# Performance work log

Hardware: AMD Instinct MI355X
Metric: run time of the kernel (lower is better)

## Reference

```python
import jax, jax.numpy as jnp
import numpy as np

NUM_HEADS = 16
HEAD_DIM = 64
NUM_BUCKETS = 32
MAX_DIST = 128
EPS = 1e-5
SCALE = HEAD_DIM ** -0.5


def layer_norm(x, g, b):
    m = jnp.mean(x, axis=-1, keepdims=True)
    v = jnp.mean(jnp.square(x - m), axis=-1, keepdims=True)
    return (x - m) * jax.lax.rsqrt(v + EPS) * g + b


def rel_pos_bias(emb, num_q, num_k):
    # T5-style relative position bucketing (non-causal, bidirectional halves)
    i, j = num_q, num_k
    q_pos = jnp.arange(j - i, j)
    k_pos = jnp.arange(j)
    rel = k_pos[None, :] - q_pos[:, None]  # [i, j]
    nb = NUM_BUCKETS // 2
    ret = (rel >= 0).astype(jnp.int32) * nb
    n = jnp.abs(rel)
    max_exact = nb // 2
    val_large = max_exact + (
        jnp.log(jnp.maximum(n, 1).astype(jnp.float32) / max_exact)
        / np.log(MAX_DIST / max_exact) * (nb - max_exact)
    ).astype(jnp.int32)
    val_large = jnp.minimum(val_large, nb - 1)
    bucket = ret + jnp.where(n < max_exact, n, val_large)
    bias = emb[bucket]                       # [i, j, h]
    return jnp.transpose(bias, (2, 0, 1))[None]  # [1, h, i, j]


def attention(x, ctx, ng, nbv, ncg, ncb, wq, wkv, wo, bo, rel_emb):
    b, n, _ = x.shape
    m = ctx.shape[1]
    xn = layer_norm(x, ng, nbv)
    cn = layer_norm(ctx, ncg, ncb)
    q = xn @ wq                              # [b, n, mid]
    kv = cn @ wkv                            # [b, m, 2*mid]
    k, v = jnp.split(kv, 2, axis=-1)
    def heads(t, L):
        return t.reshape(b, L, NUM_HEADS, HEAD_DIM).transpose(0, 2, 1, 3)
    q, k, v = heads(q, n), heads(k, m), heads(v, m)
    sim = jnp.einsum('bhnd,bhmd->bhnm', q, k)
    sim = (sim + rel_pos_bias(rel_emb, n, m)) * SCALE  # bias added pre-scale (faithful)
    attn = jax.nn.softmax(sim, axis=-1)
    out = jnp.einsum('bhnm,bhmd->bhnd', attn, v)
    out = out.transpose(0, 2, 1, 3).reshape(b, n, NUM_HEADS * HEAD_DIM)
    return out @ wo + bo


def setup_inputs() -> dict:
    key = jax.random.key(0)
    ks = jax.random.split(key, 20)
    F, MID, CF = 1024, NUM_HEADS * HEAD_DIM, 1024
    w = lambda k, shape, s=0.02: jax.random.normal(k, shape, jnp.float32) * s
    inp = {
        'x': jax.random.normal(ks[0], (2, 2048, F), jnp.float32),
        'context': jax.random.normal(ks[1], (2, 512, CF), jnp.float32),
        # self-attention params
        'sa_norm_g': 1.0 + w(ks[2], (F,), 0.1), 'sa_norm_b': w(ks[3], (F,), 0.1),
        'sa_normc_g': 1.0 + w(ks[4], (F,), 0.1), 'sa_normc_b': w(ks[5], (F,), 0.1),
        'sa_wq': w(ks[6], (F, MID)), 'sa_wkv': w(ks[7], (F, 2 * MID)),
        'sa_wo': w(ks[8], (MID, F)), 'sa_bo': w(ks[9], (F,), 0.01),
        'sa_rel': w(ks[10], (NUM_BUCKETS, NUM_HEADS), 0.1),
        # cross-attention params
        'ca_norm_g': 1.0 + w(ks[11], (F,), 0.1), 'ca_norm_b': w(ks[12], (F,), 0.1),
        'ca_normc_g': 1.0 + w(ks[13], (CF,), 0.1), 'ca_normc_b': w(ks[14], (CF,), 0.1),
        'ca_wq': w(ks[15], (F, MID)), 'ca_wkv': w(ks[16], (CF, 2 * MID)),
        'ca_wo': w(ks[17], (MID, F)), 'ca_bo': w(ks[18], (F,), 0.01),
        'ca_rel': w(ks[19], (NUM_BUCKETS, NUM_HEADS), 0.1),
    }
    return inp


def reference(x, context,
              sa_norm_g, sa_norm_b, sa_normc_g, sa_normc_b,
              sa_wq, sa_wkv, sa_wo, sa_bo, sa_rel,
              ca_norm_g, ca_norm_b, ca_normc_g, ca_normc_b,
              ca_wq, ca_wkv, ca_wo, ca_bo, ca_rel):
    # self-attention (context = x, norm_context applied to x)
    x = attention(x, x, sa_norm_g, sa_norm_b, sa_normc_g, sa_normc_b,
                  sa_wq, sa_wkv, sa_wo, sa_bo, sa_rel) + x
    # cross-attention with residual
    x = attention(x, context, ca_norm_g, ca_norm_b, ca_normc_g, ca_normc_b,
                  ca_wq, ca_wkv, ca_wo, ca_bo, ca_rel) + x
    return x
```

## Files before the change

### kernel.cpp

```cpp
#include <hip/hip_runtime.h>
#include <hip/hip_bf16.h>

typedef __hip_bfloat16 bf16;
typedef __attribute__((ext_vector_type(8))) short bf16x8;
typedef __attribute__((ext_vector_type(4))) float f32x4;

__device__ __forceinline__ float b2f(bf16 v) { return __bfloat162float(v); }
__device__ __forceinline__ bf16 f2b(float v) { return __float2bfloat16(v); }

__device__ __forceinline__ float ldx(const void* p, size_t i, bool isb) {
    return isb ? b2f(((const bf16*)p)[i]) : ((const float*)p)[i];
}
__device__ __forceinline__ void stx(void* p, size_t i, bool isb, float v) {
    if (isb) ((bf16*)p)[i] = f2b(v);
    else     ((float*)p)[i] = v;
}
__device__ __forceinline__ void ldx8(const void* p, size_t i, bool isb, float* o) {
    if (isb) {
        const bf16x8 v = *(const bf16x8*)((const bf16*)p + i);
#pragma unroll
        for (int j = 0; j < 8; j++) o[j] = b2f(((const bf16*)&v)[j]);
    } else {
        const float4 v0 = *(const float4*)((const float*)p + i);
        const float4 v1 = *(const float4*)((const float*)p + i + 4);
        o[0]=v0.x; o[1]=v0.y; o[2]=v0.z; o[3]=v0.w;
        o[4]=v1.x; o[5]=v1.y; o[6]=v1.z; o[7]=v1.w;
    }
}

__global__ void sniff_kernel(const void* __restrict__ x, int* __restrict__ flag) {
    const unsigned* w = (const unsigned*)x;
    const int t = threadIdx.x;
    int cnt = 0;
#pragma unroll
    for (int i = 0; i < 4; i++) {
        const unsigned word = w[t * 4 + i];
        const int e = (word >> 23) & 0xFF;
        cnt += (e >= 192) ? 1 : 0;
    }
    __shared__ int red[4];
#pragma unroll
    for (int o = 32; o > 0; o >>= 1) cnt += __shfl_down(cnt, o);
    if ((t & 63) == 0) red[t >> 6] = cnt;
    __syncthreads();
    if (t == 0) flag[0] = ((red[0] + red[1] + red[2] + red[3]) >= 512) ? 1 : 0;
}

__global__ void wconv4_kernel(const void* __restrict__ Wq,
                              const void* __restrict__ Wkv,
                              const void* __restrict__ Wo,
                              bf16* __restrict__ WTq, bf16* __restrict__ WTkv,
                              bf16* __restrict__ WTo,
                              const int* __restrict__ flagp) {
    const bool isb = (*flagp != 0);
    const int z = blockIdx.z;
    const void* W = (z == 0) ? Wq : (z == 3) ? Wo : Wkv;
    bf16* Wt      = (z == 0) ? WTq : (z == 3) ? WTo : WTkv;
    const int N   = (z == 1 || z == 2) ? 2048 : 1024;
    const int K = 1024;
    __shared__ float T[64][65];
    const int n0 = blockIdx.x * 64 + ((z == 2) ? 1024 : 0);
    const int k0 = blockIdx.y * 64;
    const int t = threadIdx.x;
    const int rr = t >> 3, c8 = (t & 7) * 8;
#pragma unroll
    for (int i = 0; i < 2; i++) {
        const int row = rr + i * 32;
        float v[8];
        ldx8(W, (size_t)(k0 + row) * N + n0 + c8, isb, v);
#pragma unroll
        for (int j = 0; j < 8; j++) T[row][c8 + j] = v[j];
    }
    __syncthreads();
#pragma unroll
    for (int i = 0; i < 2; i++) {
        const int row = rr + i * 32;
        bf16x8 ov;
#pragma unroll
        for (int j = 0; j < 8; j++) ((bf16*)&ov)[j] = f2b(T[c8 + j][row]);
        *(bf16x8*)(Wt + (size_t)(n0 + row) * K + k0 + c8) = ov;
    }
}

__global__ void ln_dual_kernel(const void* __restrict__ in, size_t in_off, long in_bs,
                               int in_ext,
                               const void* __restrict__ g1, const void* __restrict__ b1,
                               const void* __restrict__ g2, const void* __restrict__ b2,
                               bf16* __restrict__ out1, bf16* __restrict__ out2,
                               long out_bs, const int* __restrict__ flagp) {
    const int F = 1024;
    const bool isb = (*flagp != 0);
    const bool inb = in_ext ? isb : true;
    const int row = blockIdx.x;
    const int z = blockIdx.z;
    const int t = threadIdx.x;
    const size_t base = in_off + (size_t)z * in_bs + (size_t)row * F;
    const size_t obase = (size_t)z * out_bs + (size_t)row * F;

    float v[4];
    float s = 0.f;
#pragma unroll
    for (int i = 0; i < 4; i++) { v[i] = ldx(in, base + t + 256 * i, inb); s += v[i]; }

    __shared__ float red1[4];
    __shared__ float red2[4];
#pragma unroll
    for (int o = 32; o > 0; o >>= 1) s += __shfl_down(s, o);
    if ((t & 63) == 0) red1[t >> 6] = s;
    __syncthreads();
    const float mean = (red1[0] + red1[1] + red1[2] + red1[3]) * (1.0f / F);

    float ss = 0.f;
#pragma unroll
    for (int i = 0; i < 4; i++) { float d = v[i] - mean; ss += d * d; }
#pragma unroll
    for (int o = 32; o > 0; o >>= 1) ss += __shfl_down(ss, o);
    if ((t & 63) == 0) red2[t >> 6] = ss;
    __syncthreads();
    const float var = (red2[0] + red2[1] + red2[2] + red2[3]) * (1.0f / F);
    const float rn = rsqrtf(var + 1e-5f);

#pragma unroll
    for (int i = 0; i < 4; i++) {
        const int idx = t + 256 * i;
        const float nv = (v[i] - mean) * rn;
        out1[obase + idx] = f2b(nv * ldx(g1, idx, isb) + ldx(b1, idx, isb));
        if (out2) out2[obase + idx] = f2b(nv * ldx(g2, idx, isb) + ldx(b2, idx, isb));
    }
}

struct GArgs {
    const bf16* A; const bf16* Bt; void* C;
    const void* bias; const void* res;
    bf16* kb0; bf16* kb1;
    int c_ext, res_ext, N, mode, zsplit, zrows, nbx, nby;
};

__global__ __launch_bounds__(256) void gemm_fused(GArgs ga, GArgs gb,
                                                  const int* __restrict__ flagp) {
    const bool sec = (int)blockIdx.x >= ga.nbx;
    const GArgs g = sec ? gb : ga;
    const int bx = (int)blockIdx.x - (sec ? ga.nbx : 0);
    const int by = (int)blockIdx.y;
    if (by >= g.nby) return;

    const int K = 1024;
    const bool isb = (*flagp != 0);

    __shared__ bf16 As[128][72];
    __shared__ bf16 Bs[128][72];

    const int t = threadIdx.x;
    const int w = t >> 6, lane = t & 63, li = lane & 15, quad = lane >> 4;
    const int wm = (w & 1) * 64, wn = (w >> 1) * 64;
    const int bm = by * 128, bn = bx * 128;

    f32x4 acc[4][4];
#pragma unroll
    for (int mi = 0; mi < 4; mi++)
#pragma unroll
        for (int ni = 0; ni < 4; ni++)
#pragma unroll
            for (int r = 0; r < 4; r++) acc[mi][ni][r] = 0.f;

    for (int k0 = 0; k0 < K; k0 += 64) {
#pragma unroll
        for (int c = 0; c < 4; c++) {
            const int d = c * 256 + t;
            const int row = d >> 3, ch = (d & 7) * 8;
            *(bf16x8*)&As[row][ch] = *(const bf16x8*)(g.A + (size_t)(bm + row) * K + k0 + ch);
            *(bf16x8*)&Bs[row][ch] = *(const bf16x8*)(g.Bt + (size_t)(bn + row) * K + k0 + ch);
        }
        __syncthreads();
#pragma unroll
        for (int kc = 0; kc < 2; kc++) {
            bf16x8 af[4], bfr[4];
#pragma unroll
            for (int i = 0; i < 4; i++) {
                af[i]  = *(const bf16x8*)&As[wm + i * 16 + li][kc * 32 + quad * 8];
                bfr[i] = *(const bf16x8*)&Bs[wn + i * 16 + li][kc * 32 + quad * 8];
            }
#pragma unroll
            for (int mi = 0; mi < 4; mi++)
#pragma unroll
                for (int ni = 0; ni < 4; ni++)
                    acc[mi][ni] = __builtin_amdgcn_mfma_f32_16x16x32_bf16(
                        af[mi], bfr[ni], acc[mi][ni], 0, 0, 0);
        }
        __syncthreads();
    }

    if (g.mode == 1) {
#pragma unroll
        for (int mi = 0; mi < 4; mi++)
#pragma unroll
            for (int r = 0; r < 4; r++) {
                const int row = bm + wm + mi * 16 + quad * 4 + r;
                bf16* kb = (row < g.zsplit) ? g.kb0 : g.kb1;
                const int lrow = (row < g.zsplit) ? row : row - g.zsplit;
#pragma unroll
                for (int ni = 0; ni < 4; ni++) {
                    const int col = bn + wn + ni * 16 + li;
                    const float v = acc[mi][ni][r];
                    if (col < 1024)
                        kb[(size_t)lrow * 1024 + col] = f2b(v);
                    else
                        kb[(size_t)1024 * g.zrows + (size_t)(col - 1024) * g.zrows + lrow] = f2b(v);
                }
            }
        return;
    }

#pragma unroll
    for (int mi = 0; mi < 4; mi++)
#pragma unroll
        for (int r = 0; r < 4; r++) {
            const int row = bm + wm + mi * 16 + quad * 4 + r;
#pragma unroll
            for (int ni = 0; ni < 4; ni++) {
                const int col = bn + wn + ni * 16 + li;
                float v = acc[mi][ni][r];
                if (g.bias) v += ldx(g.bias, col, isb);
                if (g.res)  v += ldx(g.res, (size_t)row * g.N + col, g.res_ext ? isb : true);
                stx(g.C, (size_t)row * g.N + col, g.c_ext ? isb : true, v);
            }
        }
}

__global__ __launch_bounds__(256) void gemm_mfma(
    const bf16* __restrict__ A, long a_bs, const void* __restrict__ W,
    void* __restrict__ C, size_t c_off, long c_bs, int c_ext,
    const void* __restrict__ bias,
    const void* __restrict__ res, size_t res_off, long res_bs, int res_ext,
    int K, int N, int mode, int R,
    bf16* __restrict__ kb0, bf16* __restrict__ kb1,
    const int* __restrict__ flagp) {

    const bool isb = (*flagp != 0);
    const bool resb = res_ext ? isb : true;
    const bool cb = c_ext ? isb : true;
    const int z = blockIdx.z;

    const bf16* Az = A + (size_t)z * a_bs;
    const size_t coz = c_off + (size_t)z * c_bs;
    const size_t roz = res_off + (size_t)z * res_bs;

    __shared__ bf16 As[64][72];
    __shared__ bf16 Bs[64][72];

    const int t = threadIdx.x;
    const int w = t >> 6, lane = t & 63, li = lane & 15, quad = lane >> 4;
    const int wm = (w & 1) * 32, wn = (w >> 1) * 32;
    const int bm = blockIdx.y * 64, bn = blockIdx.x * 64;

    f32x4 acc[2][2];
#pragma unroll
    for (int mi = 0; mi < 2; mi++)
#pragma unroll
        for (int ni = 0; ni < 2; ni++)
#pragma unroll
            for (int r = 0; r < 4; r++) acc[mi][ni][r] = 0.f;

    for (int k0 = 0; k0 < K; k0 += 64) {
#pragma unroll
        for (int c = 0; c < 2; c++) {
            const int lin = t * 16 + c * 8;
            const int row = lin >> 6, kk = lin & 63;
            *(bf16x8*)&As[row][kk] = *(const bf16x8*)(Az + (size_t)(bm + row) * K + k0 + kk);
        }
#pragma unroll
        for (int c = 0; c < 2; c++) {
            const int lin = t * 16 + c * 8;
            const int kk = lin >> 6, n0 = lin & 63;
            float v[8];
            ldx8(W, (size_t)(k0 + kk) * N + bn + n0, isb, v);
            const int st = t & 7;
#pragma unroll
            for (int i = 0; i < 8; i++) {
                const int ii = (i + st) & 7;
                Bs[n0 + ii][kk] = f2b(v[ii]);
            }
        }
        __syncthreads();
#pragma unroll
        for (int kc = 0; kc < 2; kc++) {
            bf16x8 af[2], bfr[2];
#pragma unroll
            for (int mi = 0; mi < 2; mi++)
                af[mi] = *(const bf16x8*)&As[wm + mi * 16 + li][kc * 32 + quad * 8];
#pragma unroll
            for (int ni = 0; ni < 2; ni++)
                bfr[ni] = *(const bf16x8*)&Bs[wn + ni * 16 + li][kc * 32 + quad * 8];
#pragma unroll
            for (int mi = 0; mi < 2; mi++)
#pragma unroll
                for (int ni = 0; ni < 2; ni++)
                    acc[mi][ni] = __builtin_amdgcn_mfma_f32_16x16x32_bf16(
                        af[mi], bfr[ni], acc[mi][ni], 0, 0, 0);
        }
        __syncthreads();
    }

    if (mode == 1) {
        bf16* kb = z ? kb1 : kb0;
#pragma unroll
        for (int mi = 0; mi < 2; mi++)
#pragma unroll
            for (int r = 0; r < 4; r++) {
                const int row = bm + wm + mi * 16 + quad * 4 + r;
#pragma unroll
                for (int ni = 0; ni < 2; ni++) {
                    const int col = bn + wn + ni * 16 + li;
                    const float v = acc[mi][ni][r];
                    if (col < 1024)
                        kb[(size_t)row * 1024 + col] = f2b(v);
                    else
                        kb[(size_t)1024 * R + (size_t)(col - 1024) * R + row] = f2b(v);
                }
            }
        return;
    }

#pragma unroll
    for (int mi = 0; mi < 2; mi++)
#pragma unroll
        for (int r = 0; r < 4; r++) {
            const int row = bm + wm + mi * 16 + quad * 4 + r;
#pragma unroll
            for (int ni = 0; ni < 2; ni++) {
                const int col = bn + wn + ni * 16 + li;
                float v = acc[mi][ni][r];
                if (bias) v += ldx(bias, col, isb);
                if (res)  v += ldx(res, roz + (size_t)row * N + col, resb);
                stx(C, coz + (size_t)row * N + col, cb, v);
            }
        }
}

__global__ __launch_bounds__(64) void attn_flash(
    const bf16* __restrict__ qb, const bf16* __restrict__ kv0,
    const bf16* __restrict__ kv1,
    const void* __restrict__ rel_emb, bf16* __restrict__ out,
    long qo_bs, long out_bs, int m, int rel_off, const int* __restrict__ flagp) {

    const float SC = 0.125f * 1.44269504f;
    const bool isb = (*flagp != 0);
    const int id = blockIdx.x;
    const int xcd = id & 7;
    const int slot = id >> 3;
    const int c = (slot >> 6) * 8 + xcd;
    const int h = c & 15, z = c >> 4;
    const int q0 = (slot & 63) * 32;
    const int t = threadIdx.x;
    const int li = t & 15, quad = t >> 4;

    const bf16* qz = qb + (size_t)z * qo_bs;
    bf16* oz = out + (size_t)z * out_bs;
    const bf16* kb = z ? kv1 : kv0;
    const bf16* vtb = kb + (size_t)m * 1024;

    __shared__ float bias_s[32];
    __shared__ float tab[2080];
    __shared__ bf16 Ps[16][40];

    if (t < 32) bias_s[t] = ldx(rel_emb, t * 16 + h, isb) * SC - 40.0f;
    __syncthreads();

    const int tsz = m + 31;
    for (int i = t; i < tsz; i += 64) {
        const int rel = i - 31 - q0 + rel_off;
        const int ab = rel < 0 ? -rel : rel;
        int bucket = rel >= 0 ? 16 : 0;
        if (ab < 8) {
            bucket += ab;
        } else {
            const int p = 31 - __clz(ab);
            const int k2 = 2 * p + ((ab * ab >= (1 << (2 * p + 1))) ? 1 : 0);
            const int val = k2 + 2;
            bucket += (val > 15) ? 15 : val;
        }
        tab[i] = bias_s[bucket];
    }
    __syncthreads();

    bf16x8 aq[2][2];
#pragma unroll
    for (int g = 0; g < 2; g++)
#pragma unroll
        for (int kc = 0; kc < 2; kc++)
            aq[g][kc] = *(const bf16x8*)(qz + (size_t)(q0 + g * 16 + li) * 1024
                                         + h * 64 + kc * 32 + quad * 8);

    bf16x8 ones;
#pragma unroll
    for (int j = 0; j < 8; j++) ((short*)&ones)[j] = 0x3F80;

    f32x4 o[2][4], lac[2];
#pragma unroll
    for (int g = 0; g < 2; g++) {
#pragma unroll
        for (int r = 0; r < 4; r++) lac[g][r] = 0.f;
#pragma unroll
        for (int nb = 0; nb < 4; nb++)
#pragma unroll
            for (int r = 0; r < 4; r++) o[g][nb][r] = 0.f;
    }

#define LOADKV(KF, VF, J)                                                      \
    {                                                                          \
        _Pragma("unroll")                                                      \
        for (int nb = 0; nb < 2; nb++)                                         \
            _Pragma("unroll")                                                  \
            for (int kc = 0; kc < 2; kc++)                                     \
                KF[nb * 2 + kc] = *(const bf16x8*)(                            \
                    kb + (size_t)((J) + nb * 16 + li) * 1024 + h * 64          \
                    + kc * 32 + quad * 8);                                     \
        _Pragma("unroll")                                                      \
        for (int nb = 0; nb < 4; nb++)                                         \
            VF[nb] = *(const bf16x8*)(                                         \
                vtb + (size_t)(h * 64 + nb * 16 + li) * m + (J) + quad * 8);   \
    }

#define ABODY(KF, VF, J0)                                                      \
    {                                                                          \
        _Pragma("unroll")                                                      \
        for (int g = 0; g < 2; g++) {                                          \
            f32x4 s[2];                                                        \
            __builtin_amdgcn_s_setprio(1);                                     \
            _Pragma("unroll")                                                  \
            for (int nb = 0; nb < 2; nb++) {                                   \
                f32x4 a;                                                       \
                _Pragma("unroll")                                              \
                for (int r = 0; r < 4; r++) a[r] = 0.f;                        \
                _Pragma("unroll")                                              \
                for (int kc = 0; kc < 2; kc++)                                 \
                    a = __builtin_amdgcn_mfma_f32_16x16x32_bf16(               \
                        aq[g][kc], KF[nb * 2 + kc], a, 0, 0, 0);               \
                s[nb] = a;                                                     \
            }                                                                  \
            __builtin_amdgcn_s_setprio(0);                                     \
            _Pragma("unroll")                                                  \
            for (int nb = 0; nb < 2; nb++)                                     \
                _Pragma("unroll")                                              \
                for (int r = 0; r < 4; r++) {                                  \
                    const int ti = (J0) + nb * 16 + li + 31                    \
                                   - (g * 16 + quad * 4 + r);                  \
                    s[nb][r] = exp2f(fmaf(s[nb][r], SC, tab[ti]));             \
                }                                                              \
            _Pragma("unroll")                                                  \
            for (int nb = 0; nb < 2; nb++)                                     \
                _Pragma("unroll")                                              \
                for (int r = 0; r < 4; r++)                                    \
                    Ps[quad * 4 + r][nb * 16 + li] = f2b(s[nb][r]);            \
            const bf16x8 ap = *(const bf16x8*)&Ps[li][quad * 8];               \
            __builtin_amdgcn_s_setprio(1);                                     \
            _Pragma("unroll")                                                  \
            for (int nb = 0; nb < 4; nb++)                                     \
                o[g][nb] = __builtin_amdgcn_mfma_f32_16x16x32_bf16(            \
                    ap, VF[nb], o[g][nb], 0, 0, 0);                            \
            lac[g] = __builtin_amdgcn_mfma_f32_16x16x32_bf16(                  \
                ap, ones, lac[g], 0, 0, 0);                                    \
            __builtin_amdgcn_s_setprio(0);                                     \
        }                                                                      \
    }

    bf16x8 kA[4], vA[4], kB[4], vB[4];
    LOADKV(kA, vA, 0);
    for (int j0 = 0; j0 < m; j0 += 64) {
        LOADKV(kB, vB, j0 + 32);
        ABODY(kA, vA, j0);
        const int jn = (j0 + 64 < m) ? (j0 + 64) : 0;
        LOADKV(kA, vA, jn);
        ABODY(kB, vB, j0 + 32);
    }

#undef LOADKV
#undef ABODY

#pragma unroll
    for (int g = 0; g < 2; g++)
#pragma unroll
        for (int r = 0; r < 4; r++) {
            const float inv = 1.0f / lac[g][r];
            const int qi = q0 + g * 16 + quad * 4 + r;
#pragma unroll
            for (int nb = 0; nb < 4; nb++)
                oz[(size_t)qi * 1024 + h * 64 + nb * 16 + li] = f2b(o[g][nb][r] * inv);
        }
}

extern "C" void kernel_launch(void* const* d_in, const int* in_sizes, int n_in,
                              void* d_out, int out_size, void* d_ws, size_t ws_size,
                              hipStream_t stream) {
    const long M1 = 1024 * 1024;
    const long M2 = 2 * 1024 * 1024;
    const long M4 = 4 * 1024 * 1024;
    if (ws_size < 24u * 1024 * 1024 + 256) return;

    const void* x      = d_in[0];
    const void* ctx    = d_in[1];
    const void* sa_ng  = d_in[2];
    const void* sa_nb  = d_in[3];
    const void* sa_ncg = d_in[4];
    const void* sa_ncb = d_in[5];
    const void* sa_wq  = d_in[6];
    const void* sa_wkv = d_in[7];
    const void* sa_wo  = d_in[8];
    const void* sa_bo  = d_in[9];
    const void* sa_rel = d_in[10];
    const void* ca_ng  = d_in[11];
    const void* ca_nb  = d_in[12];
    const void* ca_ncg = d_in[13];
    const void* ca_ncb = d_in[14];
    const void* ca_wq  = d_in[15];
    const void* ca_wkv = d_in[16];
    const void* ca_wo  = d_in[17];
    const void* ca_bo  = d_in[18];
    const void* ca_rel = d_in[19];

    int* flag = (int*)d_ws;
    bf16* F_A = (bf16*)((char*)d_ws + 256);
    bf16* F_B = F_A + M4;
    bf16* F_C = F_B + M4;
    bf16* WT  = F_C + M4;
    bf16* F_X = WT + M4;
    bf16* qd  = (bf16*)d_out;

    sniff_kernel<<<1, 256, 0, stream>>>(x, flag);

    if (ws_size >= 40u * 1024 * 1024 + 256) {
        bf16* WTq = WT;
        bf16* WTkv = WT + M1;
        bf16* WTo = WT + 3 * M1;
        GArgs gz = {};

        wconv4_kernel<<<dim3(16, 16, 4), 256, 0, stream>>>(
            sa_wq, sa_wkv, sa_wo, WTq, WTkv, WTo, flag);
        ln_dual_kernel<<<dim3(2048, 1, 2), 256, 0, stream>>>(
            x, 0, M2, 1, sa_ng, sa_nb, sa_ncg, sa_ncb, F_X, F_B, M2, flag);
        {
            GArgs gq = {};
            gq.A = F_X; gq.Bt = WTq; gq.C = qd;
            gq.N = 1024; gq.nbx = 8; gq.nby = 32;
            GArgs gkv = {};
            gkv.A = F_B; gkv.Bt = WTkv;
            gkv.N = 2048; gkv.mode = 1; gkv.zsplit = 2048; gkv.zrows = 2048;
            gkv.kb0 = F_A; gkv.kb1 = F_C; gkv.nbx = 16; gkv.nby = 32;
            gemm_fused<<<dim3(24, 32), 256, 0, stream>>>(gq, gkv, flag);
        }
        attn_flash<<<dim3(2048), 64, 0, stream>>>(
            qd, F_A, F_C, sa_rel, qd, M2, M2, 2048, 0, flag);
        {
            GArgs go = {};
            go.A = qd; go.Bt = WTo; go.C = F_B;
            go.bias = sa_bo; go.res = x; go.res_ext = 1;
            go.N = 1024; go.nbx = 8; go.nby = 32;
            gemm_fused<<<dim3(8, 32), 256, 0, stream>>>(go, gz, flag);
        }

        wconv4_kernel<<<dim3(16, 16, 4), 256, 0, stream>>>(
            ca_wq, ca_wkv, ca_wo, WTq, WTkv, WTo, flag);
        ln_dual_kernel<<<dim3(2048, 1, 2), 256, 0, stream>>>(
            F_B, 0, M2, 0, ca_ng, ca_nb, nullptr, nullptr, F_X, nullptr, M2, flag);
        ln_dual_kernel<<<dim3(512, 1, 2), 256, 0, stream>>>(
            ctx, 0, 512 * 1024, 1, ca_ncg, ca_ncb, nullptr, nullptr,
            F_C, nullptr, 512 * 1024, flag);
        {
            GArgs gq = {};
            gq.A = F_X; gq.Bt = WTq; gq.C = qd;
            gq.N = 1024; gq.nbx = 8; gq.nby = 32;
            GArgs gkv = {};
            gkv.A = F_C; gkv.Bt = WTkv;
            gkv.N = 2048; gkv.mode = 1; gkv.zsplit = 512; gkv.zrows = 512;
            gkv.kb0 = F_A; gkv.kb1 = F_A + M1; gkv.nbx = 16; gkv.nby = 8;
            gemm_fused<<<dim3(24, 32), 256, 0, stream>>>(gq, gkv, flag);
        }
        attn_flash<<<dim3(2048), 64, 0, stream>>>(
            qd, F_A, F_A + M1, ca_rel, F_C, M2, M2, 512, 1536, flag);
        {
            GArgs go = {};
            go.A = F_C; go.Bt = WTo; go.C = d_out; go.c_ext = 1;
            go.bias = ca_bo; go.res = F_B;
            go.N = 1024; go.nbx = 8; go.nby = 32;
            gemm_fused<<<dim3(8, 32), 256, 0, stream>>>(go, gz, flag);
        }
        return;
    }

    ln_dual_kernel<<<dim3(2048, 1, 2), 256, 0, stream>>>(
        x, 0, M2, 1, sa_ng, sa_nb, sa_ncg, sa_ncb, F_A, F_B, M2, flag);
    gemm_mfma<<<dim3(16, 32, 2), 256, 0, stream>>>(
        F_A, M2, sa_wq, qd, 0, M2, 0, nullptr, nullptr, 0, 0, 0,
        1024, 1024, 0, 0, nullptr, nullptr, flag);
    gemm_mfma<<<dim3(32, 32, 2), 256, 0, stream>>>(
        F_B, M2, sa_wkv, nullptr, 0, 0, 0, nullptr, nullptr, 0, 0, 0,
        1024, 2048, 1, 2048, F_A, F_C, flag);
    attn_flash<<<dim3(2048), 64, 0, stream>>>(
        qd, F_A, F_C, sa_rel, qd, M2, M2, 2048, 0, flag);
    gemm_mfma<<<dim3(16, 32, 2), 256, 0, stream>>>(
        qd, M2, sa_wo, F_B, 0, M2, 0, sa_bo, x, 0, M2, 1,
        1024, 1024, 0, 0, nullptr, nullptr, flag);

    ln_dual_kernel<<<dim3(2048, 1, 2), 256, 0, stream>>>(
        F_B, 0, M2, 0, ca_ng, ca_nb, nullptr, nullptr, F_A, nullptr, M2, flag);
    ln_dual_kernel<<<dim3(512, 1, 2), 256, 0, stream>>>(
        ctx, 0, 512 * 1024, 1, ca_ncg, ca_ncb, nullptr, nullptr,
        F_C, nullptr, 512 * 1024, flag);
    gemm_mfma<<<dim3(16, 32, 2), 256, 0, stream>>>(
        F_A, M2, ca_wq, qd, 0, M2, 0, nullptr, nullptr, 0, 0, 0,
        1024, 1024, 0, 0, nullptr, nullptr, flag);
    gemm_mfma<<<dim3(32, 8, 2), 256, 0, stream>>>(
        F_C, 512 * 1024, ca_wkv, nullptr, 0, 0, 0, nullptr, nullptr, 0, 0, 0,
        1024, 2048, 1, 512, F_A, F_A + M1, flag);
    attn_flash<<<dim3(2048), 64, 0, stream>>>(
        qd, F_A, F_A + M1, ca_rel, F_C, M2, M2, 512, 1536, flag);
    gemm_mfma<<<dim3(16, 32, 2), 256, 0, stream>>>(
        F_C, M2, ca_wo, d_out, 0, M2, 1, ca_bo, F_B, 0, M2, 0,
        1024, 1024, 0, 0, nullptr, nullptr, flag);
}
```

Before: 503.0 us.

## Hoist cross-attention weight conversion and context KV projection into first phase

Both attentions' weight transposes now happen in one 8-slice conversion launch, and the context layernorm plus cross-attention K/V projection move into the first fused GEMM launch alongside the self-attention Q/KV GEMMs. This cuts kernel launches and fills the GPU better in the first GEMM, leaving a smaller Q-only GEMM for the cross phase. The attention kernel also drops s_setprio hints and double-buffers the P scratch tile per group. It needs a larger workspace (56MB threshold), and if the workspace is smaller the code falls back to the slow path.

Result: faster. 489.3 us (-2.7%).

```diff
diff --git a/kernel.cpp b/kernel.cpp
--- a/kernel.cpp
+++ b/kernel.cpp
@@ -46,20 +46,29 @@
     if (t == 0) flag[0] = ((red[0] + red[1] + red[2] + red[3]) >= 512) ? 1 : 0;
 }
 
-__global__ void wconv4_kernel(const void* __restrict__ Wq,
+__global__ void wconv8_kernel(const void* __restrict__ Wq,
                               const void* __restrict__ Wkv,
                               const void* __restrict__ Wo,
+                              const void* __restrict__ Wq2,
+                              const void* __restrict__ Wkv2,
+                              const void* __restrict__ Wo2,
                               bf16* __restrict__ WTq, bf16* __restrict__ WTkv,
                               bf16* __restrict__ WTo,
+                              bf16* __restrict__ WTq2, bf16* __restrict__ WTkv2,
+                              bf16* __restrict__ WTo2,
                               const int* __restrict__ flagp) {
     const bool isb = (*flagp != 0);
     const int z = blockIdx.z;
-    const void* W = (z == 0) ? Wq : (z == 3) ? Wo : Wkv;
-    bf16* Wt      = (z == 0) ? WTq : (z == 3) ? WTo : WTkv;
-    const int N   = (z == 1 || z == 2) ? 2048 : 1024;
+    const int zz = z & 3;
+    const bool ca = z >= 4;
+    const void* W = ca ? ((zz == 0) ? Wq2 : (zz == 3) ? Wo2 : Wkv2)
+                       : ((zz == 0) ? Wq  : (zz == 3) ? Wo  : Wkv);
+    bf16* Wt      = ca ? ((zz == 0) ? WTq2 : (zz == 3) ? WTo2 : WTkv2)
+                       : ((zz == 0) ? WTq  : (zz == 3) ? WTo  : WTkv);
+    const int N   = (zz == 1 || zz == 2) ? 2048 : 1024;
     const int K = 1024;
     __shared__ float T[64][65];
-    const int n0 = blockIdx.x * 64 + ((z == 2) ? 1024 : 0);
+    const int n0 = blockIdx.x * 64 + ((zz == 2) ? 1024 : 0);
     const int k0 = blockIdx.y * 64;
     const int t = threadIdx.x;
     const int rr = t >> 3, c8 = (t & 7) * 8;
@@ -136,11 +145,13 @@
     int c_ext, res_ext, N, mode, zsplit, zrows, nbx, nby;
 };
 
-__global__ __launch_bounds__(256) void gemm_fused(GArgs ga, GArgs gb,
+__global__ __launch_bounds__(256) void gemm_fused(GArgs ga, GArgs gb, GArgs gc,
                                                   const int* __restrict__ flagp) {
-    const bool sec = (int)blockIdx.x >= ga.nbx;
-    const GArgs g = sec ? gb : ga;
-    const int bx = (int)blockIdx.x - (sec ? ga.nbx : 0);
+    int bx = (int)blockIdx.x;
+    GArgs g;
+    if (bx < ga.nbx) { g = ga; }
+    else if (bx < ga.nbx + gb.nbx) { g = gb; bx -= ga.nbx; }
+    else { g = gc; bx -= ga.nbx + gb.nbx; }
     const int by = (int)blockIdx.y;
     if (by >= g.nby) return;
 
@@ -361,7 +372,7 @@
 
     __shared__ float bias_s[32];
     __shared__ float tab[2080];
-    __shared__ bf16 Ps[16][40];
+    __shared__ bf16 Ps[2][16][40];
 
     if (t < 32) bias_s[t] = ldx(rel_emb, t * 16 + h, isb) * SC - 40.0f;
     __syncthreads();
@@ -426,7 +437,6 @@
         _Pragma("unroll")                                                      \
         for (int g = 0; g < 2; g++) {                                          \
             f32x4 s[2];                                                        \
-            __builtin_amdgcn_s_setprio(1);                                     \
             _Pragma("unroll")                                                  \
             for (int nb = 0; nb < 2; nb++) {                                   \
                 f32x4 a;                                                       \
@@ -438,7 +448,6 @@
                         aq[g][kc], KF[nb * 2 + kc], a, 0, 0, 0);               \
                 s[nb] = a;                                                     \
             }                                                                  \
-            __builtin_amdgcn_s_setprio(0);                                     \
             _Pragma("unroll")                                                  \
             for (int nb = 0; nb < 2; nb++)                                     \
                 _Pragma("unroll")                                              \
@@ -451,16 +460,14 @@
             for (int nb = 0; nb < 2; nb++)                                     \
                 _Pragma("unroll")                                              \
                 for (int r = 0; r < 4; r++)                                    \
-                    Ps[quad * 4 + r][nb * 16 + li] = f2b(s[nb][r]);            \
-            const bf16x8 ap = *(const bf16x8*)&Ps[li][quad * 8];               \
-            __builtin_amdgcn_s_setprio(1);                                     \
+                    Ps[g][quad * 4 + r][nb * 16 + li] = f2b(s[nb][r]);         \
+            const bf16x8 ap = *(const bf16x8*)&Ps[g][li][quad * 8];            \
             _Pragma("unroll")                                                  \
             for (int nb = 0; nb < 4; nb++)                                     \
                 o[g][nb] = __builtin_amdgcn_mfma_f32_16x16x32_bf16(            \
                     ap, VF[nb], o[g][nb], 0, 0, 0);                            \
             lac[g] = __builtin_amdgcn_mfma_f32_16x16x32_bf16(                  \
                 ap, ones, lac[g], 0, 0, 0);                                    \
-            __builtin_amdgcn_s_setprio(0);                                     \
         }                                                                      \
     }
 
@@ -524,20 +531,32 @@
     bf16* F_C = F_B + M4;
     bf16* WT  = F_C + M4;
     bf16* F_X = WT + M4;
+    bf16* F_Y = F_X + M4;
+    bf16* WT2 = F_Y + 3 * M1;
     bf16* qd  = (bf16*)d_out;
 
     sniff_kernel<<<1, 256, 0, stream>>>(x, flag);
 
-    if (ws_size >= 40u * 1024 * 1024 + 256) {
-        bf16* WTq = WT;
+    if (ws_size >= 56u * 1024 * 1024 + 256) {
+        bf16* WTq  = WT;
         bf16* WTkv = WT + M1;
-        bf16* WTo = WT + 3 * M1;
+        bf16* WTo  = WT + 3 * M1;
+        bf16* WT2q  = WT2;
+        bf16* WT2kv = WT2 + M1;
+        bf16* WT2o  = WT2 + 3 * M1;
+        bf16* CAK0 = F_Y + M1;
+        bf16* CAK1 = F_Y + 2 * M1;
         GArgs gz = {};
 
-        wconv4_kernel<<<dim3(16, 16, 4), 256, 0, stream>>>(
-            sa_wq, sa_wkv, sa_wo, WTq, WTkv, WTo, flag);
+        wconv8_kernel<<<dim3(16, 16, 8), 256, 0, stream>>>(
+            sa_wq, sa_wkv, sa_wo, ca_wq, ca_wkv, ca_wo,
+            WTq, WTkv, WTo, WT2q, WT2kv, WT2o, flag);
         ln_dual_kernel<<<dim3(2048, 1, 2), 256, 0, stream>>>(
             x, 0, M2, 1, sa_ng, sa_nb, sa_ncg, sa_ncb, F_X, F_B, M2, flag);
+        ln_dual_kernel<<<dim3(512, 1, 2), 256, 0, stream>>>(
+            ctx, 0, 512 * 1024, 1, ca_ncg, ca_ncb, nullptr, nullptr,
+            F_Y, nullptr, 512 * 1024, flag);
+
         {
             GArgs gq = {};
             gq.A = F_X; gq.Bt = WTq; gq.C = qd;
@@ -546,8 +565,13 @@
             gkv.A = F_B; gkv.Bt = WTkv;
             gkv.N = 2048; gkv.mode = 1; gkv.zsplit = 2048; gkv.zrows = 2048;
             gkv.kb0 = F_A; gkv.kb1 = F_C; gkv.nbx = 16; gkv.nby = 32;
-            gemm_fused<<<dim3(24, 32), 256, 0, stream>>>(gq, gkv, flag);
-        }
+            GArgs gca = {};
+            gca.A = F_Y; gca.Bt = WT2kv;
+            gca.N = 2048; gca.mode = 1; gca.zsplit = 512; gca.zrows = 512;
+            gca.kb0 = CAK0; gca.kb1 = CAK1; gca.nbx = 16; gca.nby = 8;
+            gemm_fused<<<dim3(40, 32), 256, 0, stream>>>(gq, gkv, gca, flag);
+        }
+
         attn_flash<<<dim3(2048), 64, 0, stream>>>(
             qd, F_A, F_C, sa_rel, qd, M2, M2, 2048, 0, flag);
         {
@@ -555,34 +579,25 @@
             go.A = qd; go.Bt = WTo; go.C = F_B;
             go.bias = sa_bo; go.res = x; go.res_ext = 1;
             go.N = 1024; go.nbx = 8; go.nby = 32;
-            gemm_fused<<<dim3(8, 32), 256, 0, stream>>>(go, gz, flag);
-        }
-
-        wconv4_kernel<<<dim3(16, 16, 4), 256, 0, stream>>>(
-            ca_wq, ca_wkv, ca_wo, WTq, WTkv, WTo, flag);
+            gemm_fused<<<dim3(8, 32), 256, 0, stream>>>(go, gz, gz, flag);
+        }
+
         ln_dual_kernel<<<dim3(2048, 1, 2), 256, 0, stream>>>(
             F_B, 0, M2, 0, ca_ng, ca_nb, nullptr, nullptr, F_X, nullptr, M2, flag);
-        ln_dual_kernel<<<dim3(512, 1, 2), 256, 0, stream>>>(
-            ctx, 0, 512 * 1024, 1, ca_ncg, ca_ncb, nullptr, nullptr,
-            F_C, nullptr, 512 * 1024, flag);
         {
             GArgs gq = {};
-            gq.A = F_X; gq.Bt = WTq; gq.C = qd;
+            gq.A = F_X; gq.Bt = WT2q; gq.C = qd;
             gq.N = 1024; gq.nbx = 8; gq.nby = 32;
-            GArgs gkv = {};
-            gkv.A = F_C; gkv.Bt = WTkv;
-            gkv.N = 2048; gkv.mode = 1; gkv.zsplit = 512; gkv.zrows = 512;
-            gkv.kb0 = F_A; gkv.kb1 = F_A + M1; gkv.nbx = 16; gkv.nby = 8;
-            gemm_fused<<<dim3(24, 32), 256, 0, stream>>>(gq, gkv, flag);
+            gemm_fused<<<dim3(8, 32), 256, 0, stream>>>(gq, gz, gz, flag);
         }
         attn_flash<<<dim3(2048), 64, 0, stream>>>(
-            qd, F_A, F_A + M1, ca_rel, F_C, M2, M2, 512, 1536, flag);
+            qd, CAK0, CAK1, ca_rel, F_C, M2, M2, 512, 1536, flag);
         {
             GArgs go = {};
-            go.A = F_C; go.Bt = WTo; go.C = d_out; go.c_ext = 1;
+            go.A = F_C; go.Bt = WT2o; go.C = d_out; go.c_ext = 1;
             go.bias = ca_bo; go.res = F_B;
             go.N = 1024; go.nbx = 8; go.nby = 32;
-            gemm_fused<<<dim3(8, 32), 256, 0, stream>>>(go, gz, flag);
+            gemm_fused<<<dim3(8, 32), 256, 0, stream>>>(go, gz, gz, flag);
         }
         return;
     }
```
